# Performance work log

Measured on AMD Instinct MI355X. Metric: run time of the kernel, lower is better.

## Reference

```python
import jax, jax.numpy as jnp
import numpy as np

DEGREE = 8


def setup_inputs() -> dict:
    key = jax.random.key(0)
    k1, k2 = jax.random.split(key)
    b, c_in, c_out = 16384, 512, 512
    x = jax.random.normal(k1, (b, c_in), dtype=jnp.float32)
    std = 1.0 / (c_in * (DEGREE + 1))
    cheby_coeffs = jax.random.normal(k2, (c_in, c_out, DEGREE + 1), dtype=jnp.float32) * std
    return {"x": x, "cheby_coeffs": cheby_coeffs}


def reference(x, cheby_coeffs):
    # x: (b, c_in); cheby_coeffs: (c_in, c_out, degree+1)
    arange = jnp.arange(DEGREE + 1, dtype=x.dtype)  # (d+1,)
    # double tanh squashes into (-1, 1), then Chebyshev basis via acos/cos
    t = jnp.arccos(jnp.tanh(jnp.tanh(x)))            # (b, c_in)
    basis = jnp.cos(t[:, :, None] * arange)          # (b, c_in, d+1)
    y = jnp.einsum('bid,iod->bo', basis, cheby_coeffs)
    return y
```

## Files before the change

kernel.cpp:

```cpp
#include <hip/hip_runtime.h>
#include <hip/hip_bf16.h>
#include <stdint.h>

#define CIN   512
#define COUT  512
#define BM    128
#define BN    256
#define NIB   16
#define KSTEPS 128

typedef float f32x4 __attribute__((ext_vector_type(4)));
typedef short s16x8 __attribute__((ext_vector_type(8)));

__device__ uint4 Wp_g[KSTEPS * 32 * 64];
__device__ float bias_g[COUT];

__device__ __forceinline__ uint32_t cvtpk(float lo, float hi) {
  uint32_t r;
  asm("v_cvt_pk_bf16_f32 %0, %1, %2" : "=v"(r) : "v"(lo), "v"(hi));
  return r;
}

__device__ __forceinline__ float ftanh(float v) {
  float e = __expf(v + v);
  return 1.0f - __fdividef(2.0f, e + 1.0f);
}

__global__ void pack_w(const float* __restrict__ cw) {
  __shared__ float lf[32 * 144];
  int ib = blockIdx.x >> 5;
  int cg = blockIdx.x & 31;
  for (int r = threadIdx.x; r < 32 * 144; r += 256) {
    int il = r / 144;
    int rem = r - il * 144;
    lf[r] = cw[(size_t)(ib * 32 + il) * (COUT * 9) + cg * 144 + rem];
  }
  __syncthreads();
  for (int v = threadIdx.x; v < 512; v += 256) {
    int ksl = v >> 6;
    int lane = v & 63;
    int d = ksl + 1;
    int lh = lane >> 4, l15 = lane & 15;
    uint32_t p[4];
    #pragma unroll
    for (int q = 0; q < 4; ++q) {
      float a = lf[(lh * 8 + 2 * q    ) * 144 + l15 * 9 + d];
      float b = lf[(lh * 8 + 2 * q + 1) * 144 + l15 * 9 + d];
      p[q] = cvtpk(a, b);
    }
    Wp_g[((ib * 8 + ksl) * 32 + cg) * 64 + lane] = make_uint4(p[0], p[1], p[2], p[3]);
  }
}

__global__ void bias_k(const float* __restrict__ cw) {
  int o = blockIdx.x;
  int t = threadIdx.x;
  float s = 0.f;
  #pragma unroll
  for (int q = 0; q < 8; ++q)
    s += cw[(size_t)(t + 64 * q) * (COUT * 9) + o * 9];
  #pragma unroll
  for (int off = 32; off; off >>= 1) s += __shfl_down(s, off);
  if (t == 0) bias_g[o] = s;
}

__global__ void __launch_bounds__(512, 2) cheby_gemm(const float* __restrict__ x,
                                                     float* __restrict__ out) {
  __shared__ uint4 lds[2 * 4 * 4 * BM];
  const int tid  = threadIdx.x;
  const int lane = tid & 63;
  const int l15  = lane & 15;
  const int lh   = lane >> 4;
  const int w    = tid >> 6;
  const int wr   = w >> 2;
  const int wc   = w & 3;

  int b0  = blockIdx.x;
  int bid = (b0 & 7) * 32 + (b0 >> 3);
  const int rb  = (bid >> 1) * BM;
  const int cb  = bid & 1;
  const int ocb = cb * BN;
  const int cgbase = cb * 16 + wc * 4;

  const int ge   = w >> 1;
  const int grow = (w & 1) * 64 + lane;
  const float* xrow = x + (size_t)(rb + grow) * CIN + ge * 8;

  f32x4 acc[4][4];
  #pragma unroll
  for (int cf = 0; cf < 4; ++cf) {
    float bv = bias_g[ocb + wc * 64 + cf * 16 + l15];
    #pragma unroll
    for (int rf = 0; rf < 4; ++rf) {
      acc[rf][cf][0] = bv; acc[rf][cf][1] = bv;
      acc[rf][cf][2] = bv; acc[rf][cf][3] = bv;
    }
  }

  float xv[8], u2[8], tm1[8], tm2[8];

  auto loadX = [&](int ib) {
    const float4* p = reinterpret_cast<const float4*>(xrow + ib * 32);
    float4 v0 = p[0], v1 = p[1];
    xv[0] = v0.x; xv[1] = v0.y; xv[2] = v0.z; xv[3] = v0.w;
    xv[4] = v1.x; xv[5] = v1.y; xv[6] = v1.z; xv[7] = v1.w;
  };
  auto compute_u = [&]() {
    #pragma unroll
    for (int k = 0; k < 8; ++k) {
      float u = ftanh(ftanh(xv[k]));
      tm1[k] = u; tm2[k] = 1.0f; u2[k] = u + u;
    }
  };
  auto advance = [&]() {
    #pragma unroll
    for (int k = 0; k < 8; ++k) {
      float t = __builtin_fmaf(u2[k], tm1[k], -tm2[k]);
      tm2[k] = tm1[k]; tm1[k] = t;
    }
  };
  auto emit = [&](int buf, int slot) {
    uint32_t p0 = cvtpk(tm1[0], tm1[1]);
    uint32_t p1 = cvtpk(tm1[2], tm1[3]);
    uint32_t p2 = cvtpk(tm1[4], tm1[5]);
    uint32_t p3 = cvtpk(tm1[6], tm1[7]);
    lds[((buf * 4 + slot) * 4 + ge) * BM + grow] = make_uint4(p0, p1, p2, p3);
  };

  s16x8 bcur[4], bnxt[4];
  auto loadB = [&](s16x8* dst, int ks) {
    #pragma unroll
    for (int cf = 0; cf < 4; ++cf) {
      uint4 v = Wp_g[(ks * 32 + cgbase + cf) * 64 + lane];
      dst[cf] = __builtin_bit_cast(s16x8, v);
    }
  };
  auto mfma_step = [&](int buf, int slot) {
    s16x8 a[4];
    int base = ((buf * 4 + slot) * 4 + lh) * BM + wr * 64 + l15;
    #pragma unroll
    for (int rf = 0; rf < 4; ++rf)
      a[rf] = *reinterpret_cast<const s16x8*>(&lds[base + rf * 16]);
    #pragma unroll
    for (int rf = 0; rf < 4; ++rf) {
      #pragma unroll
      for (int cf = 0; cf < 4; ++cf)
        acc[rf][cf] = __builtin_amdgcn_mfma_f32_16x16x32_bf16(
            a[rf], bcur[cf], acc[rf][cf], 0, 0, 0);
    }
  };

  loadX(0);
  compute_u();
  emit(0, 0);
  advance(); emit(0, 1);
  advance(); emit(0, 2);
  advance(); emit(0, 3);
  loadB(bcur, 0);
  __syncthreads();

  for (int ib = 0; ib < NIB; ++ib) {
    if (ib + 1 < NIB) loadX(ib + 1);

    #pragma unroll
    for (int j = 0; j < 4; ++j) {
      int ks = ib * 8 + j;
      loadB(bnxt, ks + 1);
      mfma_step(0, j);
      advance(); emit(1, j);
      #pragma unroll
      for (int cf = 0; cf < 4; ++cf) bcur[cf] = bnxt[cf];
    }
    __syncthreads();

    #pragma unroll
    for (int j = 0; j < 4; ++j) {
      int ks = ib * 8 + 4 + j;
      if (ks + 1 < KSTEPS) loadB(bnxt, ks + 1);
      mfma_step(1, j);
      if (ib + 1 < NIB) {
        if (j == 0) { compute_u(); emit(0, 0); }
        else        { advance();   emit(0, j); }
      }
      #pragma unroll
      for (int cf = 0; cf < 4; ++cf) bcur[cf] = bnxt[cf];
    }
    __syncthreads();
  }

  const int orow = rb + wr * 64 + lh * 4;
  const int ocol = ocb + wc * 64 + l15;
  #pragma unroll
  for (int rf = 0; rf < 4; ++rf) {
    #pragma unroll
    for (int cf = 0; cf < 4; ++cf) {
      #pragma unroll
      for (int r = 0; r < 4; ++r)
        out[(size_t)(orow + rf * 16 + r) * COUT + ocol + cf * 16] = acc[rf][cf][r];
    }
  }
}

extern "C" void kernel_launch(void* const* d_in, const int* in_sizes, int n_in,
                              void* d_out, int out_size, void* d_ws, size_t ws_size,
                              hipStream_t stream) {
  const float* x  = (const float*)d_in[0];
  const float* cw = (const float*)d_in[1];
  float* out = (float*)d_out;

  pack_w<<<dim3(512), dim3(256), 0, stream>>>(cw);
  bias_k<<<dim3(COUT), dim3(64), 0, stream>>>(cw);
  cheby_gemm<<<dim3(256), dim3(512), 0, stream>>>(x, out);
}
```

Baseline: 91.18 us.

## Split GEMM block into 16 waves with dedicated basis-generator waves

Doubles the block to 1024 threads (16 waves), halving each wave's output columns so the accumulator tile shrinks from 4x4 to 4x2 fragments. Only the first 8 waves generate the Chebyshev basis into LDS, and all waves run MFMA. B fragments are now double-buffered by parity instead of copied, and the MFMA section runs under raised s_setprio. The aim is more waves per CU to hide latency and lower register pressure, at the cost of more B-fragment loads per output and uneven work between generator and non-generator waves.

Result: slower. 94.40 us (+3.5%).

```diff
diff --git a/kernel.cpp b/kernel.cpp
--- a/kernel.cpp
+++ b/kernel.cpp
@@ -64,32 +64,35 @@
   if (t == 0) bias_g[o] = s;
 }
 
-__global__ void __launch_bounds__(512, 2) cheby_gemm(const float* __restrict__ x,
-                                                     float* __restrict__ out) {
+__global__ void __launch_bounds__(1024, 4) cheby_gemm(const float* __restrict__ x,
+                                                      float* __restrict__ out) {
   __shared__ uint4 lds[2 * 4 * 4 * BM];
   const int tid  = threadIdx.x;
   const int lane = tid & 63;
   const int l15  = lane & 15;
   const int lh   = lane >> 4;
   const int w    = tid >> 6;
-  const int wr   = w >> 2;
-  const int wc   = w & 3;
+  const int wr   = w >> 3;
+  const int wc   = w & 7;
+  const bool genw = (w < 8);
 
   int b0  = blockIdx.x;
   int bid = (b0 & 7) * 32 + (b0 >> 3);
   const int rb  = (bid >> 1) * BM;
   const int cb  = bid & 1;
   const int ocb = cb * BN;
-  const int cgbase = cb * 16 + wc * 4;
-
-  const int ge   = w >> 1;
+  const int cgbase = cb * 16 + wc * 2;
+
+  const int ge   = (w & 7) >> 1;
   const int grow = (w & 1) * 64 + lane;
   const float* xrow = x + (size_t)(rb + grow) * CIN + ge * 8;
 
-  f32x4 acc[4][4];
-  #pragma unroll
-  for (int cf = 0; cf < 4; ++cf) {
-    float bv = bias_g[ocb + wc * 64 + cf * 16 + l15];
+  const uint4* pB = Wp_g + (size_t)cgbase * 64 + lane;
+
+  f32x4 acc[4][2];
+  #pragma unroll
+  for (int cf = 0; cf < 2; ++cf) {
+    float bv = bias_g[ocb + wc * 32 + cf * 16 + l15];
     #pragma unroll
     for (int rf = 0; rf < 4; ++rf) {
       acc[rf][cf][0] = bv; acc[rf][cf][1] = bv;
@@ -127,73 +130,73 @@
     lds[((buf * 4 + slot) * 4 + ge) * BM + grow] = make_uint4(p0, p1, p2, p3);
   };
 
-  s16x8 bcur[4], bnxt[4];
-  auto loadB = [&](s16x8* dst, int ks) {
-    #pragma unroll
-    for (int cf = 0; cf < 4; ++cf) {
-      uint4 v = Wp_g[(ks * 32 + cgbase + cf) * 64 + lane];
-      dst[cf] = __builtin_bit_cast(s16x8, v);
-    }
-  };
-  auto mfma_step = [&](int buf, int slot) {
+  s16x8 breg[2][2];
+  auto loadB = [&](int par, int ks) {
+    #pragma unroll
+    for (int cf = 0; cf < 2; ++cf) {
+      uint4 v = pB[(size_t)ks * 2048 + cf * 64];
+      breg[par][cf] = __builtin_bit_cast(s16x8, v);
+    }
+  };
+  auto mfma_step = [&](int buf, int slot, int par) {
     s16x8 a[4];
     int base = ((buf * 4 + slot) * 4 + lh) * BM + wr * 64 + l15;
     #pragma unroll
     for (int rf = 0; rf < 4; ++rf)
       a[rf] = *reinterpret_cast<const s16x8*>(&lds[base + rf * 16]);
+    __builtin_amdgcn_s_setprio(1);
     #pragma unroll
     for (int rf = 0; rf < 4; ++rf) {
       #pragma unroll
-      for (int cf = 0; cf < 4; ++cf)
+      for (int cf = 0; cf < 2; ++cf)
         acc[rf][cf] = __builtin_amdgcn_mfma_f32_16x16x32_bf16(
-            a[rf], bcur[cf], acc[rf][cf], 0, 0, 0);
-    }
-  };
-
-  loadX(0);
-  compute_u();
-  emit(0, 0);
-  advance(); emit(0, 1);
-  advance(); emit(0, 2);
-  advance(); emit(0, 3);
-  loadB(bcur, 0);
+            a[rf], breg[par][cf], acc[rf][cf], 0, 0, 0);
+    }
+    __builtin_amdgcn_s_setprio(0);
+  };
+
+  if (genw) {
+    loadX(0);
+    compute_u();
+    emit(0, 0);
+    advance(); emit(0, 1);
+    advance(); emit(0, 2);
+    advance(); emit(0, 3);
+  }
+  loadB(0, 0);
   __syncthreads();
 
   for (int ib = 0; ib < NIB; ++ib) {
-    if (ib + 1 < NIB) loadX(ib + 1);
+    if (genw && ib + 1 < NIB) loadX(ib + 1);
 
     #pragma unroll
     for (int j = 0; j < 4; ++j) {
       int ks = ib * 8 + j;
-      loadB(bnxt, ks + 1);
-      mfma_step(0, j);
-      advance(); emit(1, j);
-      #pragma unroll
-      for (int cf = 0; cf < 4; ++cf) bcur[cf] = bnxt[cf];
+      loadB((j + 1) & 1, ks + 1);
+      mfma_step(0, j, j & 1);
+      if (genw) { advance(); emit(1, j); }
     }
     __syncthreads();
 
     #pragma unroll
     for (int j = 0; j < 4; ++j) {
       int ks = ib * 8 + 4 + j;
-      if (ks + 1 < KSTEPS) loadB(bnxt, ks + 1);
-      mfma_step(1, j);
-      if (ib + 1 < NIB) {
+      if (ks + 1 < KSTEPS) loadB((j + 1) & 1, ks + 1);
+      mfma_step(1, j, j & 1);
+      if (genw && ib + 1 < NIB) {
         if (j == 0) { compute_u(); emit(0, 0); }
         else        { advance();   emit(0, j); }
       }
-      #pragma unroll
-      for (int cf = 0; cf < 4; ++cf) bcur[cf] = bnxt[cf];
     }
     __syncthreads();
   }
 
   const int orow = rb + wr * 64 + lh * 4;
-  const int ocol = ocb + wc * 64 + l15;
+  const int ocol = ocb + wc * 32 + l15;
   #pragma unroll
   for (int rf = 0; rf < 4; ++rf) {
     #pragma unroll
-    for (int cf = 0; cf < 4; ++cf) {
+    for (int cf = 0; cf < 2; ++cf) {
       #pragma unroll
       for (int r = 0; r < 4; ++r)
         out[(size_t)(orow + rf * 16 + r) * COUT + ocol + cf * 16] = acc[rf][cf][r];
@@ -210,5 +213,5 @@
 
   pack_w<<<dim3(512), dim3(256), 0, stream>>>(cw);
   bias_k<<<dim3(COUT), dim3(64), 0, stream>>>(cw);
-  cheby_gemm<<<dim3(256), dim3(512), 0, stream>>>(x, out);
-}
+  cheby_gemm<<<dim3(256), dim3(1024), 0, stream>>>(x, out);
+}
```

## Build Chebyshev A-fragments in registers, dropping LDS staging and barriers

Applied to the files above, without the earlier changes.

Each lane now loads the x values for the rows and columns it needs as an MFMA A-operand and computes the tanh/Chebyshev recurrence in registers. The shared-memory staging buffer and the __syncthreads barriers are removed. Because the A-fragment is no longer shared across the 4 column waves, each wave recomputes the basis for its own rows, and the tanh and recurrence work is done twice over the k-dimension (once per row pair). B fragments are double-buffered in registers, x is prefetched, and s_setprio brackets the MFMA blocks. The exchange is more redundant VALU work and register pressure for no LDS traffic or barrier stalls.

Measured after the change: 152.7 us. 1.67x slower.

```diff
diff --git a/kernel.cpp b/kernel.cpp
--- a/kernel.cpp
+++ b/kernel.cpp
@@ -4,8 +4,6 @@
 
 #define CIN   512
 #define COUT  512
-#define BM    128
-#define BN    256
 #define NIB   16
 #define KSTEPS 128
 
@@ -66,7 +64,6 @@
 
 __global__ void __launch_bounds__(512, 2) cheby_gemm(const float* __restrict__ x,
                                                      float* __restrict__ out) {
-  __shared__ uint4 lds[2 * 4 * 4 * BM];
   const int tid  = threadIdx.x;
   const int lane = tid & 63;
   const int l15  = lane & 15;
@@ -77,14 +74,14 @@
 
   int b0  = blockIdx.x;
   int bid = (b0 & 7) * 32 + (b0 >> 3);
-  const int rb  = (bid >> 1) * BM;
+  const int rb  = (bid >> 1) * 128;
   const int cb  = bid & 1;
-  const int ocb = cb * BN;
+  const int ocb = cb * 256;
   const int cgbase = cb * 16 + wc * 4;
 
-  const int ge   = w >> 1;
-  const int grow = (w & 1) * 64 + lane;
-  const float* xrow = x + (size_t)(rb + grow) * CIN + ge * 8;
+  const uint4* pB = Wp_g + (size_t)cgbase * 64 + lane;
+
+  const float* xbase = x + (size_t)(rb + wr * 64 + l15) * CIN + lh * 8;
 
   f32x4 acc[4][4];
   #pragma unroll
@@ -97,95 +94,77 @@
     }
   }
 
-  float xv[8], u2[8], tm1[8], tm2[8];
+  float xbufA[16], xbufB[16];
+  float u2[16], tm1[16], tm2[16];
 
-  auto loadX = [&](int ib) {
-    const float4* p = reinterpret_cast<const float4*>(xrow + ib * 32);
-    float4 v0 = p[0], v1 = p[1];
-    xv[0] = v0.x; xv[1] = v0.y; xv[2] = v0.z; xv[3] = v0.w;
-    xv[4] = v1.x; xv[5] = v1.y; xv[6] = v1.z; xv[7] = v1.w;
+  auto prefetch_to = [&](float* dst, int qq) {
+    int ibq = qq >> 1, pq = qq & 1;
+    #pragma unroll
+    for (int rl = 0; rl < 2; ++rl) {
+      const float4* p4 = reinterpret_cast<const float4*>(
+          xbase + (size_t)(pq * 2 + rl) * 16 * CIN + ibq * 32);
+      float4 a = p4[0], b = p4[1];
+      dst[rl*8+0]=a.x; dst[rl*8+1]=a.y; dst[rl*8+2]=a.z; dst[rl*8+3]=a.w;
+      dst[rl*8+4]=b.x; dst[rl*8+5]=b.y; dst[rl*8+6]=b.z; dst[rl*8+7]=b.w;
+    }
   };
-  auto compute_u = [&]() {
+  auto compute_u = [&](const float* src) {
     #pragma unroll
-    for (int k = 0; k < 8; ++k) {
-      float u = ftanh(ftanh(xv[k]));
-      tm1[k] = u; tm2[k] = 1.0f; u2[k] = u + u;
+    for (int c = 0; c < 16; ++c) {
+      float u = ftanh(ftanh(src[c]));
+      tm1[c] = u; tm2[c] = 1.0f; u2[c] = u + u;
     }
   };
   auto advance = [&]() {
     #pragma unroll
-    for (int k = 0; k < 8; ++k) {
-      float t = __builtin_fmaf(u2[k], tm1[k], -tm2[k]);
-      tm2[k] = tm1[k]; tm1[k] = t;
-    }
-  };
-  auto emit = [&](int buf, int slot) {
-    uint32_t p0 = cvtpk(tm1[0], tm1[1]);
-    uint32_t p1 = cvtpk(tm1[2], tm1[3]);
-    uint32_t p2 = cvtpk(tm1[4], tm1[5]);
-    uint32_t p3 = cvtpk(tm1[6], tm1[7]);
-    lds[((buf * 4 + slot) * 4 + ge) * BM + grow] = make_uint4(p0, p1, p2, p3);
-  };
-
-  s16x8 bcur[4], bnxt[4];
-  auto loadB = [&](s16x8* dst, int ks) {
-    #pragma unroll
-    for (int cf = 0; cf < 4; ++cf) {
-      uint4 v = Wp_g[(ks * 32 + cgbase + cf) * 64 + lane];
-      dst[cf] = __builtin_bit_cast(s16x8, v);
-    }
-  };
-  auto mfma_step = [&](int buf, int slot) {
-    s16x8 a[4];
-    int base = ((buf * 4 + slot) * 4 + lh) * BM + wr * 64 + l15;
-    #pragma unroll
-    for (int rf = 0; rf < 4; ++rf)
-      a[rf] = *reinterpret_cast<const s16x8*>(&lds[base + rf * 16]);
-    #pragma unroll
-    for (int rf = 0; rf < 4; ++rf) {
-      #pragma unroll
-      for (int cf = 0; cf < 4; ++cf)
-        acc[rf][cf] = __builtin_amdgcn_mfma_f32_16x16x32_bf16(
-            a[rf], bcur[cf], acc[rf][cf], 0, 0, 0);
+    for (int c = 0; c < 16; ++c) {
+      float t = __builtin_fmaf(u2[c], tm1[c], -tm2[c]);
+      tm2[c] = tm1[c]; tm1[c] = t;
     }
   };
 
-  loadX(0);
-  compute_u();
-  emit(0, 0);
-  advance(); emit(0, 1);
-  advance(); emit(0, 2);
-  advance(); emit(0, 3);
-  loadB(bcur, 0);
-  __syncthreads();
+  s16x8 breg[2][4];
+  auto loadB = [&](int par, int ks) {
+    #pragma unroll
+    for (int cf = 0; cf < 4; ++cf) {
+      uint4 v = pB[(size_t)ks * 2048 + cf * 64];
+      breg[par][cf] = __builtin_bit_cast(s16x8, v);
+    }
+  };
+
+  prefetch_to(xbufA, 0);
+  loadB(0, 0);
 
   for (int ib = 0; ib < NIB; ++ib) {
-    if (ib + 1 < NIB) loadX(ib + 1);
-
     #pragma unroll
-    for (int j = 0; j < 4; ++j) {
-      int ks = ib * 8 + j;
-      loadB(bnxt, ks + 1);
-      mfma_step(0, j);
-      advance(); emit(1, j);
+    for (int p = 0; p < 2; ++p) {
+      const float* src = p ? xbufB : xbufA;
+      float*       nxt = p ? xbufA : xbufB;
+      compute_u(src);
+      if (!(ib == NIB - 1 && p == 1))
+        prefetch_to(nxt, ib * 2 + p + 1);
       #pragma unroll
-      for (int cf = 0; cf < 4; ++cf) bcur[cf] = bnxt[cf];
+      for (int j = 0; j < 8; ++j) {
+        int ks = ib * 8 + j;
+        int nks = (j < 7) ? ks + 1 : ((p == 0) ? ib * 8 : (ib + 1) * 8);
+        if (!(ib == NIB - 1 && p == 1 && j == 7)) loadB((j + 1) & 1, nks);
+        if (j > 0) advance();
+        __builtin_amdgcn_s_setprio(1);
+        #pragma unroll
+        for (int rl = 0; rl < 2; ++rl) {
+          uint32_t q0 = cvtpk(tm1[rl*8+0], tm1[rl*8+1]);
+          uint32_t q1 = cvtpk(tm1[rl*8+2], tm1[rl*8+3]);
+          uint32_t q2 = cvtpk(tm1[rl*8+4], tm1[rl*8+5]);
+          uint32_t q3 = cvtpk(tm1[rl*8+6], tm1[rl*8+7]);
+          s16x8 af = __builtin_bit_cast(s16x8, make_uint4(q0, q1, q2, q3));
+          #pragma unroll
+          for (int cf = 0; cf < 4; ++cf)
+            acc[p * 2 + rl][cf] = __builtin_amdgcn_mfma_f32_16x16x32_bf16(
+                af, breg[j & 1][cf], acc[p * 2 + rl][cf], 0, 0, 0);
+        }
+        __builtin_amdgcn_s_setprio(0);
+      }
     }
-    __syncthreads();
-
-    #pragma unroll
-    for (int j = 0; j < 4; ++j) {
-      int ks = ib * 8 + 4 + j;
-      if (ks + 1 < KSTEPS) loadB(bnxt, ks + 1);
-      mfma_step(1, j);
-      if (ib + 1 < NIB) {
-        if (j == 0) { compute_u(); emit(0, 0); }
-        else        { advance();   emit(0, j); }
-      }
-      #pragma unroll
-      for (int cf = 0; cf < 4; ++cf) bcur[cf] = bnxt[cf];
-    }
-    __syncthreads();
   }
 
   const int orow = rb + wr * 64 + lh * 4;
```

## Software-pipeline LDS A-fragment reads and double-buffer B registers with per-step barriers

Applied to the files above, without the earlier changes.

Restructures the GEMM main loop so the A fragments for the next k-step are read from LDS into alternating register sets while the current step's MFMAs run. B fragments now go into two register sets indexed by parity, which removes the register copies. Each k-step is bracketed by an explicit lgkmcnt wait plus s_barrier, and the MFMA block runs under raised s_setprio. Launch bounds drop to one block per CU so the extra live registers fit. The cost is more barriers per tile, and the kernel relies on the single-block occupancy being enough to hide the Chebyshev basis generation.

Result: slower. 101.2 us (+11.0%).

```diff
diff --git a/kernel.cpp b/kernel.cpp
--- a/kernel.cpp
+++ b/kernel.cpp
@@ -64,7 +64,7 @@
   if (t == 0) bias_g[o] = s;
 }
 
-__global__ void __launch_bounds__(512, 2) cheby_gemm(const float* __restrict__ x,
+__global__ void __launch_bounds__(512, 1) cheby_gemm(const float* __restrict__ x,
                                                      float* __restrict__ out) {
   __shared__ uint4 lds[2 * 4 * 4 * BM];
   const int tid  = threadIdx.x;
@@ -86,6 +86,8 @@
   const int grow = (w & 1) * 64 + lane;
   const float* xrow = x + (size_t)(rb + grow) * CIN + ge * 8;
 
+  const uint4* pB = Wp_g + (size_t)cgbase * 64 + lane;
+
   f32x4 acc[4][4];
   #pragma unroll
   for (int cf = 0; cf < 4; ++cf) {
@@ -127,27 +129,37 @@
     lds[((buf * 4 + slot) * 4 + ge) * BM + grow] = make_uint4(p0, p1, p2, p3);
   };
 
-  s16x8 bcur[4], bnxt[4];
-  auto loadB = [&](s16x8* dst, int ks) {
+  s16x8 aA[4], aB[4];
+  s16x8 breg[2][4];
+  auto loadB = [&](int par, int ks) {
     #pragma unroll
     for (int cf = 0; cf < 4; ++cf) {
-      uint4 v = Wp_g[(ks * 32 + cgbase + cf) * 64 + lane];
-      dst[cf] = __builtin_bit_cast(s16x8, v);
-    }
-  };
-  auto mfma_step = [&](int buf, int slot) {
-    s16x8 a[4];
+      uint4 v = pB[(size_t)ks * 2048 + cf * 64];
+      breg[par][cf] = __builtin_bit_cast(s16x8, v);
+    }
+  };
+  auto dsreadA = [&](s16x8 (&dst)[4], int buf, int slot) {
     int base = ((buf * 4 + slot) * 4 + lh) * BM + wr * 64 + l15;
     #pragma unroll
     for (int rf = 0; rf < 4; ++rf)
-      a[rf] = *reinterpret_cast<const s16x8*>(&lds[base + rf * 16]);
+      dst[rf] = *reinterpret_cast<const s16x8*>(&lds[base + rf * 16]);
+  };
+  auto barrier_pre = [&]() {
+    asm volatile("s_waitcnt lgkmcnt(0)" ::: "memory");
+    __builtin_amdgcn_sched_barrier(0);
+    __builtin_amdgcn_s_barrier();
+  };
+  auto mfma16 = [&](s16x8 (&a)[4], int par) {
+    __builtin_amdgcn_s_setprio(1);
     #pragma unroll
     for (int rf = 0; rf < 4; ++rf) {
       #pragma unroll
       for (int cf = 0; cf < 4; ++cf)
         acc[rf][cf] = __builtin_amdgcn_mfma_f32_16x16x32_bf16(
-            a[rf], bcur[cf], acc[rf][cf], 0, 0, 0);
-    }
+            a[rf], breg[par][cf], acc[rf][cf], 0, 0, 0);
+    }
+    __builtin_amdgcn_s_setprio(0);
+    __builtin_amdgcn_s_barrier();
   };
 
   loadX(0);
@@ -156,8 +168,9 @@
   advance(); emit(0, 1);
   advance(); emit(0, 2);
   advance(); emit(0, 3);
-  loadB(bcur, 0);
-  __syncthreads();
+  loadB(0, 0);
+  barrier_pre();
+  dsreadA(aA, 0, 0);
 
   for (int ib = 0; ib < NIB; ++ib) {
     if (ib + 1 < NIB) loadX(ib + 1);
@@ -165,27 +178,27 @@
     #pragma unroll
     for (int j = 0; j < 4; ++j) {
       int ks = ib * 8 + j;
-      loadB(bnxt, ks + 1);
-      mfma_step(0, j);
+      if (j < 3) { if (j & 1) dsreadA(aA, 0, j + 1); else dsreadA(aB, 0, j + 1); }
+      else       dsreadA(aA, 1, 0);
+      loadB((j + 1) & 1, ks + 1);
       advance(); emit(1, j);
-      #pragma unroll
-      for (int cf = 0; cf < 4; ++cf) bcur[cf] = bnxt[cf];
-    }
-    __syncthreads();
+      barrier_pre();
+      if (j & 1) mfma16(aB, 1); else mfma16(aA, 0);
+    }
 
     #pragma unroll
     for (int j = 0; j < 4; ++j) {
       int ks = ib * 8 + 4 + j;
-      if (ks + 1 < KSTEPS) loadB(bnxt, ks + 1);
-      mfma_step(1, j);
+      if (j < 3) { if (j & 1) dsreadA(aA, 1, j + 1); else dsreadA(aB, 1, j + 1); }
+      else if (ib + 1 < NIB) dsreadA(aA, 0, 0);
+      if (ks + 1 < KSTEPS) loadB((j + 1) & 1, ks + 1);
       if (ib + 1 < NIB) {
         if (j == 0) { compute_u(); emit(0, 0); }
         else        { advance();   emit(0, j); }
       }
-      #pragma unroll
-      for (int cf = 0; cf < 4; ++cf) bcur[cf] = bnxt[cf];
-    }
-    __syncthreads();
+      barrier_pre();
+      if (j & 1) mfma16(aB, 1); else mfma16(aA, 0);
+    }
   }
 
   const int orow = rb + wr * 64 + lh * 4;
```
